# Optimization experiments

Measured on AMD Instinct MI355X. Metric: run time of the kernel, lower is better.

Reference implementation:

```python
import jax, jax.numpy as jnp
import numpy as np

B, T, E = 2, 512, 1024        # batch, max_tokens, embedding dim
S, A = 2048, 30               # num_spans, max_arg_span


def setup_inputs() -> dict:
    key = jax.random.key(0)
    k1, k2, k3, k4 = jax.random.split(key, 4)
    x = jax.random.normal(k1, (B, T, E), dtype=jnp.float32)
    W = jax.random.normal(k2, (E, 1), dtype=jnp.float32) * (1.0 / np.sqrt(E))
    b = jnp.zeros((1,), dtype=jnp.float32)
    start = jax.random.randint(k3, (S,), 0, T, dtype=jnp.int32)
    width = jax.random.randint(k4, (S,), 1, A + 1, dtype=jnp.int32)
    end = jnp.minimum(start + width - 1, T - 1).astype(jnp.int32)
    return {"x": x, "W": W, "b": b, "start": start, "end": end}


def reference(x, W, b, start, end):
    # span_indices: clamp start+offset to last token, shape [S, A]
    span_idx = jnp.minimum(jnp.arange(A)[None, :] + start[:, None], T - 1)
    # gather span token embeddings: [B, S, A, E]
    span_emb = x[:, span_idx, :]
    # tiny per-token head score: Dense(1, relu) -> [B, T, 1]
    head_scores = jax.nn.relu(x @ W + b)
    # validity mask over span positions (log-mask), [S, A]
    span_width = end - start + 1
    valid = jnp.arange(A)[None, :] < span_width[:, None]
    log_mask = jnp.where(valid, 0.0, -jnp.inf)
    # gather scores per span position, add log-mask: [B, S, A, 1]
    span_head = head_scores[:, span_idx, :] + log_mask[None, :, :, None]
    # softmax over span-position axis (axis=2)
    attn = jax.nn.softmax(span_head, axis=2)
    # weighted-sum pooling over span positions -> [B, S, E]
    return jnp.sum(span_emb * attn, axis=2)
```

## Files before the change

### kernel.cpp

```cpp
#include <hip/hip_runtime.h>
#include <math.h>

#define TT 512
#define EE 1024
#define AA 30

typedef float f32x4 __attribute__((ext_vector_type(4)));

__global__ __launch_bounds__(256) void head_kernel(const float* __restrict__ x,
                                                   const float* __restrict__ W,
                                                   const float* __restrict__ bias,
                                                   float* __restrict__ head, int BT) {
    int row  = blockIdx.x * 4 + (threadIdx.x >> 6);
    int lane = threadIdx.x & 63;
    if (row >= BT) return;
    const f32x4* xr = reinterpret_cast<const f32x4*>(x + (size_t)row * EE);
    const f32x4* wr = reinterpret_cast<const f32x4*>(W);
    float acc = 0.f;
    #pragma unroll
    for (int i = lane; i < EE / 4; i += 64) {
        f32x4 xv = xr[i];
        f32x4 wv = wr[i];
        acc += xv.x * wv.x + xv.y * wv.y + xv.z * wv.z + xv.w * wv.w;
    }
    #pragma unroll
    for (int off = 32; off; off >>= 1) acc += __shfl_xor(acc, off, 64);
    if (lane == 0) head[row] = fmaxf(acc + bias[0], 0.0f);
}

template <int SWZ>
__global__ __launch_bounds__(256) void span_kernel(const float* __restrict__ x,
                                                   const float* __restrict__ head,
                                                   const int* __restrict__ start,
                                                   const int* __restrict__ end,
                                                   float* __restrict__ out, int S) {
    int bid = blockIdx.x;
    int b, s;
    if (SWZ) {
        int xcd = bid & 7;
        b = xcd >> 2;
        s = ((bid >> 3) << 2) + (xcd & 3);
    } else {
        b = bid / S;
        s = bid - b * S;
    }

    int st = start[s];
    int wd = end[s] - st + 1;
    int nA = wd < AA ? wd : AA;

    __shared__ float wts[AA];
    int tid = threadIdx.x;

    if (tid < 64) {
        int a = tid;
        bool valid = (a < nA);
        int idx = st + a; if (idx > TT - 1) idx = TT - 1;
        float sc = valid ? head[b * TT + idx] : -INFINITY;
        float m = sc;
        #pragma unroll
        for (int off = 32; off; off >>= 1) m = fmaxf(m, __shfl_xor(m, off, 64));
        float e = valid ? __expf(sc - m) : 0.0f;
        float sum = e;
        #pragma unroll
        for (int off = 32; off; off >>= 1) sum += __shfl_xor(sum, off, 64);
        if (valid) wts[a] = e / sum;
    }
    __syncthreads();

    const f32x4* xb = reinterpret_cast<const f32x4*>(x + (size_t)b * TT * EE);
    int e4 = tid;
    f32x4 acc = (f32x4)(0.f);
    for (int a = 0; a < nA; ++a) {
        float w = wts[a];
        int idx = st + a;
        f32x4 v = xb[(size_t)idx * (EE / 4) + e4];
        acc += w * v;
    }
    f32x4* op = reinterpret_cast<f32x4*>(out) + (size_t)(b * S + s) * (EE / 4) + e4;
    __builtin_nontemporal_store(acc, op);
}

extern "C" void kernel_launch(void* const* d_in, const int* in_sizes, int n_in,
                              void* d_out, int out_size, void* d_ws, size_t ws_size,
                              hipStream_t stream) {
    const float* x     = (const float*)d_in[0];
    const float* W     = (const float*)d_in[1];
    const float* bias  = (const float*)d_in[2];
    const int*   start = (const int*)d_in[3];
    const int*   end   = (const int*)d_in[4];
    float*       out   = (float*)d_out;

    const int BT = in_sizes[0] / EE;
    const int S  = in_sizes[3];
    const int B  = BT / TT;

    float* head = (float*)d_ws;

    head_kernel<<<(BT + 3) / 4, 256, 0, stream>>>(x, W, bias, head, BT);
    if (B == 2 && (S & 3) == 0) {
        span_kernel<1><<<B * S, 256, 0, stream>>>(x, head, start, end, out, S);
    } else {
        span_kernel<0><<<B * S, 256, 0, stream>>>(x, head, start, end, out, S);
    }
}
```

Before: 22.59 us.

## Gather spans from a bf16 copy of x written by the head kernel

The head kernel now also writes a bf16 (round-to-nearest-even) copy of x into workspace. A new span kernel gathers from that half-size copy and handles two spans per block, 128 threads each with 8 elements per thread. The aim is to halve gather read bytes and cut block count. This reduces input precision to bf16, drops the XCD swizzle, and adds an extra 2 MB write in the head kernel.

```diff
diff --git a/kernel.cpp b/kernel.cpp
--- a/kernel.cpp
+++ b/kernel.cpp
@@ -7,51 +7,104 @@
 
 typedef float f32x4 __attribute__((ext_vector_type(4)));
 
+__device__ __forceinline__ unsigned bf16rne(float f) {
+    unsigned u = __float_as_uint(f);
+    return (u + 0x7fffu + ((u >> 16) & 1u)) >> 16;
+}
+__device__ __forceinline__ float blo(unsigned u) { return __uint_as_float(u << 16); }
+__device__ __forceinline__ float bhi(unsigned u) { return __uint_as_float(u & 0xffff0000u); }
+
 __global__ __launch_bounds__(256) void head_kernel(const float* __restrict__ x,
                                                    const float* __restrict__ W,
                                                    const float* __restrict__ bias,
-                                                   float* __restrict__ head, int BT) {
+                                                   float* __restrict__ head,
+                                                   ushort* __restrict__ x16, int BT) {
     int row  = blockIdx.x * 4 + (threadIdx.x >> 6);
     int lane = threadIdx.x & 63;
     if (row >= BT) return;
     const f32x4* xr = reinterpret_cast<const f32x4*>(x + (size_t)row * EE);
     const f32x4* wr = reinterpret_cast<const f32x4*>(W);
+    uint2* cr = reinterpret_cast<uint2*>(x16 + (size_t)row * EE);
     float acc = 0.f;
     #pragma unroll
-    for (int i = lane; i < EE / 4; i += 64) {
+    for (int k = 0; k < 4; ++k) {
+        int i = lane + 64 * k;
         f32x4 xv = xr[i];
         f32x4 wv = wr[i];
         acc += xv.x * wv.x + xv.y * wv.y + xv.z * wv.z + xv.w * wv.w;
+        if (x16) {
+            uint2 pk;
+            pk.x = bf16rne(xv.x) | (bf16rne(xv.y) << 16);
+            pk.y = bf16rne(xv.z) | (bf16rne(xv.w) << 16);
+            cr[i] = pk;
+        }
     }
     #pragma unroll
     for (int off = 32; off; off >>= 1) acc += __shfl_xor(acc, off, 64);
     if (lane == 0) head[row] = fmaxf(acc + bias[0], 0.0f);
 }
 
-template <int SWZ>
+__global__ __launch_bounds__(256) void span16_kernel(const ushort* __restrict__ x16,
+                                                     const float* __restrict__ head,
+                                                     const int* __restrict__ start,
+                                                     const int* __restrict__ end,
+                                                     float* __restrict__ out, int S) {
+    int p = blockIdx.x;
+    __shared__ float wts[2][AA];
+
+    int wv = threadIdx.x >> 6, l64 = threadIdx.x & 63;
+    if (wv < 2) {
+        int gg = 2 * p + wv;
+        int bb = gg / S, ss = gg - bb * S;
+        int st0 = start[ss];
+        int nA0 = min(end[ss] - st0 + 1, AA);
+        bool valid = l64 < nA0;
+        int idx = st0 + l64; if (idx > TT - 1) idx = TT - 1;
+        float sc = valid ? head[bb * TT + idx] : -INFINITY;
+        float m = sc;
+        #pragma unroll
+        for (int off = 32; off; off >>= 1) m = fmaxf(m, __shfl_xor(m, off, 64));
+        float e = valid ? __expf(sc - m) : 0.0f;
+        float sum = e;
+        #pragma unroll
+        for (int off = 32; off; off >>= 1) sum += __shfl_xor(sum, off, 64);
+        if (valid) wts[wv][l64] = e / sum;
+    }
+    __syncthreads();
+
+    int sp   = threadIdx.x >> 7;
+    int lane = threadIdx.x & 127;
+    int gg = 2 * p + sp;
+    int b = gg / S, s = gg - b * S;
+    int st = start[s];
+    int nA = min(end[s] - st + 1, AA);
+
+    const uint4* xr = reinterpret_cast<const uint4*>(x16 + (size_t)b * TT * EE);
+    f32x4 acc0 = (f32x4)(0.f), acc1 = (f32x4)(0.f);
+    for (int a = 0; a < nA; ++a) {
+        float w = wts[sp][a];
+        uint4 v = xr[(size_t)(st + a) * (EE / 8) + lane];
+        acc0.x += w * blo(v.x); acc0.y += w * bhi(v.x);
+        acc0.z += w * blo(v.y); acc0.w += w * bhi(v.y);
+        acc1.x += w * blo(v.z); acc1.y += w * bhi(v.z);
+        acc1.z += w * blo(v.w); acc1.w += w * bhi(v.w);
+    }
+    f32x4* op = reinterpret_cast<f32x4*>(out) + (size_t)gg * (EE / 4) + 2 * lane;
+    __builtin_nontemporal_store(acc0, op);
+    __builtin_nontemporal_store(acc1, op + 1);
+}
+
 __global__ __launch_bounds__(256) void span_kernel(const float* __restrict__ x,
                                                    const float* __restrict__ head,
                                                    const int* __restrict__ start,
                                                    const int* __restrict__ end,
                                                    float* __restrict__ out, int S) {
-    int bid = blockIdx.x;
-    int b, s;
-    if (SWZ) {
-        int xcd = bid & 7;
-        b = xcd >> 2;
-        s = ((bid >> 3) << 2) + (xcd & 3);
-    } else {
-        b = bid / S;
-        s = bid - b * S;
-    }
-
+    int bs = blockIdx.x;
+    int b = bs / S, s = bs - b * S;
     int st = start[s];
-    int wd = end[s] - st + 1;
-    int nA = wd < AA ? wd : AA;
-
+    int nA = min(end[s] - st + 1, AA);
     __shared__ float wts[AA];
     int tid = threadIdx.x;
-
     if (tid < 64) {
         int a = tid;
         bool valid = (a < nA);
@@ -67,17 +120,12 @@
         if (valid) wts[a] = e / sum;
     }
     __syncthreads();
-
     const f32x4* xb = reinterpret_cast<const f32x4*>(x + (size_t)b * TT * EE);
-    int e4 = tid;
     f32x4 acc = (f32x4)(0.f);
     for (int a = 0; a < nA; ++a) {
-        float w = wts[a];
-        int idx = st + a;
-        f32x4 v = xb[(size_t)idx * (EE / 4) + e4];
-        acc += w * v;
+        acc += wts[a] * xb[(size_t)(st + a) * (EE / 4) + tid];
     }
-    f32x4* op = reinterpret_cast<f32x4*>(out) + (size_t)(b * S + s) * (EE / 4) + e4;
+    f32x4* op = reinterpret_cast<f32x4*>(out) + (size_t)bs * (EE / 4) + tid;
     __builtin_nontemporal_store(acc, op);
 }
 
@@ -95,12 +143,14 @@
     const int S  = in_sizes[3];
     const int B  = BT / TT;
 
-    float* head = (float*)d_ws;
+    float*  head = (float*)d_ws;
+    size_t  need = 8192 + (size_t)BT * EE * sizeof(ushort);
+    ushort* x16  = (ws_size >= need) ? (ushort*)((char*)d_ws + 8192) : nullptr;
 
-    head_kernel<<<(BT + 3) / 4, 256, 0, stream>>>(x, W, bias, head, BT);
-    if (B == 2 && (S & 3) == 0) {
-        span_kernel<1><<<B * S, 256, 0, stream>>>(x, head, start, end, out, S);
+    head_kernel<<<(BT + 3) / 4, 256, 0, stream>>>(x, W, bias, head, x16, BT);
+    if (x16 && (S & 1) == 0) {
+        span16_kernel<<<B * S / 2, 256, 0, stream>>>(x16, head, start, end, out, S);
     } else {
-        span_kernel<0><<<B * S, 256, 0, stream>>>(x, head, start, end, out, S);
+        span_kernel<<<B * S, 256, 0, stream>>>(x, head, start, end, out, S);
     }
 }
```

Result: faster. 20.93 us (-7.4%).

## Fuse head scoring into span pooling with one wave per span

Applied to the files above, without the earlier changes.

Removes the separate head-score kernel. Each wavefront now handles one span: it computes the relu(x·W+b) score for each span token on the fly, then accumulates exp-weighted rows with an online sum and normalizes once at the end. This drops the extra launch, the head workspace round-trip, the shared-memory weights and the block barrier. In exchange it recomputes token dot products redundantly across overlapping spans, and it skips max-subtraction in the softmax, which relies on the scores staying small.

```diff
diff --git a/kernel.cpp b/kernel.cpp
--- a/kernel.cpp
+++ b/kernel.cpp
@@ -7,78 +7,87 @@
 
 typedef float f32x4 __attribute__((ext_vector_type(4)));
 
-__global__ __launch_bounds__(256) void head_kernel(const float* __restrict__ x,
-                                                   const float* __restrict__ W,
-                                                   const float* __restrict__ bias,
-                                                   float* __restrict__ head, int BT) {
-    int row  = blockIdx.x * 4 + (threadIdx.x >> 6);
-    int lane = threadIdx.x & 63;
-    if (row >= BT) return;
-    const f32x4* xr = reinterpret_cast<const f32x4*>(x + (size_t)row * EE);
-    const f32x4* wr = reinterpret_cast<const f32x4*>(W);
-    float acc = 0.f;
-    #pragma unroll
-    for (int i = lane; i < EE / 4; i += 64) {
-        f32x4 xv = xr[i];
-        f32x4 wv = wr[i];
-        acc += xv.x * wv.x + xv.y * wv.y + xv.z * wv.z + xv.w * wv.w;
-    }
-    #pragma unroll
-    for (int off = 32; off; off >>= 1) acc += __shfl_xor(acc, off, 64);
-    if (lane == 0) head[row] = fmaxf(acc + bias[0], 0.0f);
+static __device__ __forceinline__ float dot4(f32x4 p, f32x4 q) {
+    return p.x * q.x + p.y * q.y + p.z * q.z + p.w * q.w;
 }
 
 template <int SWZ>
-__global__ __launch_bounds__(256) void span_kernel(const float* __restrict__ x,
-                                                   const float* __restrict__ head,
-                                                   const int* __restrict__ start,
-                                                   const int* __restrict__ end,
-                                                   float* __restrict__ out, int S) {
-    int bid = blockIdx.x;
-    int b, s;
+__global__ __launch_bounds__(256) void fused_span_kernel(const float* __restrict__ x,
+                                                         const float* __restrict__ W,
+                                                         const float* __restrict__ bias,
+                                                         const int* __restrict__ start,
+                                                         const int* __restrict__ end,
+                                                         float* __restrict__ out,
+                                                         int S, int G) {
+    int bid  = blockIdx.x;
+    int wv   = threadIdx.x >> 6;
+    int lane = threadIdx.x & 63;
+    int b, s, g;
     if (SWZ) {
         int xcd = bid & 7;
         b = xcd >> 2;
-        s = ((bid >> 3) << 2) + (xcd & 3);
+        int local = ((bid >> 3) << 2) | (xcd & 3);
+        s = local * 4 + wv;
+        g = b * S + s;
     } else {
-        b = bid / S;
-        s = bid - b * S;
+        g = bid * 4 + wv;
+        if (g >= G) return;
+        b = g / S;
+        s = g - b * S;
     }
 
     int st = start[s];
-    int wd = end[s] - st + 1;
-    int nA = wd < AA ? wd : AA;
+    int nA = min(end[s] - st + 1, AA);
 
-    __shared__ float wts[AA];
-    int tid = threadIdx.x;
+    const f32x4* xb = reinterpret_cast<const f32x4*>(x + ((size_t)b * TT + st) * EE) + lane;
+    const f32x4* wp = reinterpret_cast<const f32x4*>(W) + lane;
 
-    if (tid < 64) {
-        int a = tid;
-        bool valid = (a < nA);
-        int idx = st + a; if (idx > TT - 1) idx = TT - 1;
-        float sc = valid ? head[b * TT + idx] : -INFINITY;
-        float m = sc;
+    f32x4 w0 = wp[0], w1 = wp[64], w2 = wp[128], w3 = wp[192];
+    f32x4 a0 = (f32x4)(0.f), a1 = (f32x4)(0.f), a2 = (f32x4)(0.f), a3 = (f32x4)(0.f);
+    float sum = 0.f;
+    float bsc = bias[0];
+
+    int a = 0;
+    for (; a + 2 <= nA; a += 2) {
+        const f32x4* r0 = xb + (size_t)a * (EE / 4);
+        const f32x4* r1 = r0 + (EE / 4);
+        f32x4 v0 = r0[0], v1 = r0[64], v2 = r0[128], v3 = r0[192];
+        f32x4 u0 = r1[0], u1 = r1[64], u2 = r1[128], u3 = r1[192];
+        float d0 = dot4(v0, w0) + dot4(v1, w1) + dot4(v2, w2) + dot4(v3, w3);
+        float d1 = dot4(u0, w0) + dot4(u1, w1) + dot4(u2, w2) + dot4(u3, w3);
         #pragma unroll
-        for (int off = 32; off; off >>= 1) m = fmaxf(m, __shfl_xor(m, off, 64));
-        float e = valid ? __expf(sc - m) : 0.0f;
-        float sum = e;
+        for (int off = 32; off; off >>= 1) {
+            d0 += __shfl_xor(d0, off, 64);
+            d1 += __shfl_xor(d1, off, 64);
+        }
+        float p0 = __expf(fmaxf(d0 + bsc, 0.f));
+        float p1 = __expf(fmaxf(d1 + bsc, 0.f));
+        sum += p0 + p1;
+        a0 += p0 * v0 + p1 * u0;
+        a1 += p0 * v1 + p1 * u1;
+        a2 += p0 * v2 + p1 * u2;
+        a3 += p0 * v3 + p1 * u3;
+    }
+    if (a < nA) {
+        const f32x4* r0 = xb + (size_t)a * (EE / 4);
+        f32x4 v0 = r0[0], v1 = r0[64], v2 = r0[128], v3 = r0[192];
+        float d0 = dot4(v0, w0) + dot4(v1, w1) + dot4(v2, w2) + dot4(v3, w3);
         #pragma unroll
-        for (int off = 32; off; off >>= 1) sum += __shfl_xor(sum, off, 64);
-        if (valid) wts[a] = e / sum;
+        for (int off = 32; off; off >>= 1) d0 += __shfl_xor(d0, off, 64);
+        float p0 = __expf(fmaxf(d0 + bsc, 0.f));
+        sum += p0;
+        a0 += p0 * v0;
+        a1 += p0 * v1;
+        a2 += p0 * v2;
+        a3 += p0 * v3;
     }
-    __syncthreads();
 
-    const f32x4* xb = reinterpret_cast<const f32x4*>(x + (size_t)b * TT * EE);
-    int e4 = tid;
-    f32x4 acc = (f32x4)(0.f);
-    for (int a = 0; a < nA; ++a) {
-        float w = wts[a];
-        int idx = st + a;
-        f32x4 v = xb[(size_t)idx * (EE / 4) + e4];
-        acc += w * v;
-    }
-    f32x4* op = reinterpret_cast<f32x4*>(out) + (size_t)(b * S + s) * (EE / 4) + e4;
-    __builtin_nontemporal_store(acc, op);
+    float inv = 1.0f / sum;
+    f32x4* op = reinterpret_cast<f32x4*>(out + (size_t)g * EE) + lane;
+    __builtin_nontemporal_store(a0 * inv, op);
+    __builtin_nontemporal_store(a1 * inv, op + 64);
+    __builtin_nontemporal_store(a2 * inv, op + 128);
+    __builtin_nontemporal_store(a3 * inv, op + 192);
 }
 
 extern "C" void kernel_launch(void* const* d_in, const int* in_sizes, int n_in,
@@ -94,13 +103,11 @@
     const int BT = in_sizes[0] / EE;
     const int S  = in_sizes[3];
     const int B  = BT / TT;
+    const int G  = B * S;
 
-    float* head = (float*)d_ws;
-
-    head_kernel<<<(BT + 3) / 4, 256, 0, stream>>>(x, W, bias, head, BT);
-    if (B == 2 && (S & 3) == 0) {
-        span_kernel<1><<<B * S, 256, 0, stream>>>(x, head, start, end, out, S);
+    if (B == 2 && S == 2048) {
+        fused_span_kernel<1><<<G / 4, 256, 0, stream>>>(x, W, bias, start, end, out, S, G);
     } else {
-        span_kernel<0><<<B * S, 256, 0, stream>>>(x, head, start, end, out, S);
+        fused_span_kernel<0><<<(G + 3) / 4, 256, 0, stream>>>(x, W, bias, start, end, out, S, G);
     }
 }
```

New measurement: 19.55 us, median of 2. 1.16x faster.
